# Performance work log

Measured on AMD Instinct MI355X. Metric: run time of the kernel, lower is better.

The kernel has to match this reference:

```python
import jax, jax.numpy as jnp
import numpy as np

EMBED_DIM = 1024
ATTN_DIM = 1024


def setup_inputs() -> dict:
    key = jax.random.key(0)
    k1, k2, k3, k4 = jax.random.split(key, 4)
    embedded = jax.random.normal(k1, (4, 2048, EMBED_DIM), dtype=jnp.float32)
    # torch nn.Linear weights are [out_features, in_features]
    s = 1.0 / np.sqrt(EMBED_DIM)
    Wk = jax.random.uniform(k2, (ATTN_DIM, EMBED_DIM), jnp.float32, -s, s)
    Wq = jax.random.uniform(k3, (ATTN_DIM, EMBED_DIM), jnp.float32, -s, s)
    Wv = jax.random.uniform(k4, (ATTN_DIM, EMBED_DIM), jnp.float32, -s, s)
    return {"embedded": embedded, "Wk": Wk, "Wq": Wq, "Wv": Wv}


def reference(embedded, Wk, Wq, Wv):
    # projections: x @ W.T  (torch Linear, no bias)
    k = jnp.einsum("bse,ae->bsa", embedded, Wk)
    q = jnp.einsum("bse,ae->bsa", embedded, Wq)
    v = jnp.einsum("bse,ae->bsa", embedded, Wv)
    scale = 1.0 / jnp.sqrt(jnp.float32(ATTN_DIM))
    attn = jnp.einsum("bqa,bka->bqk", q, k) * scale  # [B, S, S]
    S = attn.shape[1]
    causal = jnp.tril(jnp.ones((S, S), dtype=bool))
    attn = jnp.where(causal[None, :, :], attn, -jnp.inf)
    a = jax.nn.softmax(attn, axis=2)
    out = jnp.einsum("bqk,bka->bqa", a, v)
    return jnp.round(out, 4)
```

## Files before the change

### kernel.cpp

```cpp
#include <hip/hip_runtime.h>
#include <hip/hip_bf16.h>
#include <stdint.h>

typedef __bf16 bf16_t;
typedef bf16_t bf16x8 __attribute__((ext_vector_type(8)));
typedef bf16_t bf16x4 __attribute__((ext_vector_type(4)));
typedef float f32x4 __attribute__((ext_vector_type(4)));

#define BM 128
#define BN 128
#define BK 32

__device__ __forceinline__ void gload_lds16(const void* g, void* l) {
    __builtin_amdgcn_global_load_lds(
        (const __attribute__((address_space(1))) void*)(uintptr_t)g,
        (__attribute__((address_space(3))) void*)(uintptr_t)l,
        16, 0, 0);
}

template <int EPI>
__device__ __forceinline__ void gemm_body(
    bf16_t* __restrict__ As, bf16_t* __restrict__ Bs,
    const bf16_t* __restrict__ A, long lda,
    const bf16_t* __restrict__ B, long ldb,
    void* __restrict__ Cv, long ldc,
    int k0beg, int k1end, float scale, int m0, int n0,
    float* __restrict__ rs, int use_atomic)
{
    const int tid = threadIdx.x;
    const int wid = tid >> 6, lane = tid & 63;
    const int wr = wid >> 1, wc = wid & 1;
    const int hw = lane >> 4, ln = lane & 15;

    const bf16_t *srcA[2], *srcB[2];
#pragma unroll
    for (int i = 0; i < 2; i++) {
        const int c = tid + i * 256;
        const int row = c >> 2;
        const int j = ((c & 3) - (row >> 1)) & 3;
        srcA[i] = A + (size_t)(m0 + row) * lda + j * 8;
        srcB[i] = B + (size_t)(n0 + row) * ldb + j * 8;
    }

    f32x4 acc[4][4] = {};

    for (int k0 = k0beg; k0 < k1end; k0 += BK) {
        gload_lds16(srcA[0] + k0, &As[wid * 512]);
        gload_lds16(srcA[1] + k0, &As[2048 + wid * 512]);
        gload_lds16(srcB[0] + k0, &Bs[wid * 512]);
        gload_lds16(srcB[1] + k0, &Bs[2048 + wid * 512]);
        __syncthreads();

        bf16x8 af[4], bfr[4];
#pragma unroll
        for (int t = 0; t < 4; t++) {
            const int r  = wr * 64 + t * 16 + ln;
            const int rb = wc * 64 + t * 16 + ln;
            af[t]  = *(const bf16x8*)&As[r  * BK + (((hw + (r  >> 1)) & 3) * 8)];
            bfr[t] = *(const bf16x8*)&Bs[rb * BK + (((hw + (rb >> 1)) & 3) * 8)];
        }
#pragma unroll
        for (int ti = 0; ti < 4; ti++)
#pragma unroll
            for (int tj = 0; tj < 4; tj++)
                acc[ti][tj] = __builtin_amdgcn_mfma_f32_16x16x32_bf16(
                    af[ti], bfr[tj], acc[ti][tj], 0, 0, 0);
        __syncthreads();
    }

#pragma unroll
    for (int ti = 0; ti < 4; ti++) {
        const int rbase = m0 + wr * 64 + ti * 16 + hw * 4;
        f32x4 inv4;
        if (EPI == 2) {
            const float4 r4 = *(const float4*)&rs[rbase];
            inv4[0] = 1.0f / r4.x; inv4[1] = 1.0f / r4.y;
            inv4[2] = 1.0f / r4.z; inv4[3] = 1.0f / r4.w;
        }
        float part[4] = {0.f, 0.f, 0.f, 0.f};
#pragma unroll
        for (int tj = 0; tj < 4; tj++) {
            const int col = n0 + wc * 64 + tj * 16 + ln;
            if (EPI == 4) {
                const int bb = rbase >> 11;
                const int s  = rbase & 2047;
                const int d  = col - 2048;
                bf16x4 o;
#pragma unroll
                for (int rg = 0; rg < 4; rg++) o[rg] = (bf16_t)acc[ti][tj][rg];
                *(bf16x4*)&((bf16_t*)Cv)[(size_t)bb * 2097152 + (size_t)d * 2048 + s] = o;
            } else {
#pragma unroll
                for (int rg = 0; rg < 4; rg++) {
                    const size_t idx = (size_t)(rbase + rg) * ldc + col;
                    if (EPI == 0) {
                        ((bf16_t*)Cv)[idx] = (bf16_t)(acc[ti][tj][rg]);
                    } else if (EPI == 2) {
                        const float v = acc[ti][tj][rg] * inv4[rg];
                        if (use_atomic) atomicAdd(&((float*)Cv)[idx], v);
                        else            ((float*)Cv)[idx] = v;
                    } else {
                        const float e = (col <= rbase + rg)
                                      ? __expf(acc[ti][tj][rg] * scale) : 0.0f;
                        part[rg] += e;
                        ((bf16_t*)Cv)[idx] = (bf16_t)e;
                    }
                }
            }
        }
        if (EPI == 3) {
#pragma unroll
            for (int rg = 0; rg < 4; rg++) {
                float p = part[rg];
                p += __shfl_xor(p, 1, 64);
                p += __shfl_xor(p, 2, 64);
                p += __shfl_xor(p, 4, 64);
                p += __shfl_xor(p, 8, 64);
                if (ln == 0) atomicAdd(&rs[rbase + rg], p);
            }
        }
    }
}

__global__ __launch_bounds__(256) void gemm1_qkv(
    const bf16_t* __restrict__ xb, const bf16_t* __restrict__ Wb,
    bf16_t* __restrict__ QKVb, bf16_t* __restrict__ Vt)
{
    __shared__ __align__(16) bf16_t As[BM * BK];
    __shared__ __align__(16) bf16_t Bs[BN * BK];
    const int lin = blockIdx.x;
    const int xcd = lin & 7;
    const int j   = lin >> 3;
    const int p   = j >> 6;
    const int w   = j & 63;
    const int mblk = xcd * 8 + (w >> 3);
    const int nblk = p * 8 + (w & 7);
    const int m0 = mblk * BM, n0 = nblk * BN;
    if (nblk < 16)
        gemm_body<0>(As, Bs, xb, 1024, Wb, 1024, QKVb, 2048,
                     0, 1024, 1.0f, m0, n0, nullptr, 0);
    else
        gemm_body<4>(As, Bs, xb, 1024, Wb, 1024, Vt, 2048,
                     0, 1024, 1.0f, m0, n0, nullptr, 0);
}

__global__ __launch_bounds__(256) void qk_gemm(
    const bf16_t* __restrict__ QKVb, bf16_t* __restrict__ E,
    float* __restrict__ rowsum)
{
    __shared__ __align__(16) bf16_t As[BM * BK];
    __shared__ __align__(16) bf16_t Bs[BN * BK];
    const int b = blockIdx.x & 3;
    int rem = blockIdx.x >> 2;
    int my = 15, nx = 0;
#pragma unroll
    for (int m = 15; m >= 0; --m) {
        if (rem < m + 1) { my = m; nx = rem; break; }
        rem -= m + 1;
    }
    const bf16_t* base = QKVb + (size_t)b * (2048L * 2048);
    gemm_body<3>(As, Bs,
                 base + 1024, 2048,
                 base, 2048,
                 E + (size_t)b * (2048L * 2048), 2048,
                 0, 1024, 0.03125f, my * BM, nx * BN,
                 rowsum + b * 2048, 0);
}

__global__ __launch_bounds__(256) void gemm3_pv(
    const bf16_t* __restrict__ E, const bf16_t* __restrict__ Vt,
    const float* __restrict__ rowsum, float* __restrict__ out)
{
    __shared__ __align__(16) bf16_t As[BM * BK];
    __shared__ __align__(16) bf16_t Bs[BN * BK];
    const int b = blockIdx.x & 3;
    const int item = blockIdx.x >> 2;
    int s, nx, k0, k1, at;
    if (item < 64) {
        s = item >> 3; nx = item & 7;
        k0 = 0; k1 = (s + 1) * 128; at = 0;
    } else {
        const int q = item - 64;
        s = 8 + (q >> 4);
        const int r = q & 15;
        const int ci = r >> 3;
        nx = r & 7;
        k0 = ci ? 1024 : 0;
        k1 = ci ? (s + 1) * 128 : 1024;
        at = 1;
    }
    gemm_body<2>(As, Bs,
                 E + (size_t)b * (2048L * 2048), 2048,
                 Vt + (size_t)b * (1024L * 2048), 2048,
                 out + (size_t)b * (2048L * 1024), 1024,
                 k0, k1, 1.0f, s * BM, nx * BN,
                 (float*)rowsum + b * 2048, at);
}

__global__ __launch_bounds__(256) void cast_all(
    const float* __restrict__ x,
    const float* __restrict__ Wk, const float* __restrict__ Wq,
    const float* __restrict__ Wv,
    bf16_t* __restrict__ xb, bf16_t* __restrict__ Wb,
    float* __restrict__ rowsum, float* __restrict__ out)
{
    const int blk = blockIdx.x;
    if (blk >= 11272) {
        const int v = blk - 11272;
        const size_t off = (size_t)(v >> 10) * 2097152 + 1048576
                         + (size_t)(v & 1023) * 1024 + (size_t)threadIdx.x * 4;
        *(float4*)(out + off) = make_float4(0.f, 0.f, 0.f, 0.f);
        return;
    }
    if (blk >= 11264) {
        const size_t i = ((size_t)(blk - 11264) * 256 + threadIdx.x) * 4;
        *(float4*)(rowsum + i) = make_float4(0.f, 0.f, 0.f, 0.f);
        return;
    }
    const float* src;
    bf16_t* dst;
    if (blk < 8192) {
        const size_t i = ((size_t)blk * 256 + threadIdx.x) * 4;
        src = x + i;
        dst = xb + i;
    } else {
        const size_t j = ((size_t)(blk - 8192) * 256 + threadIdx.x) * 4;
        dst = Wb + j;
        if (j < (size_t)1048576)      src = Wk + j;
        else if (j < (size_t)2097152) src = Wq + (j - 1048576);
        else                          src = Wv + (j - 2097152);
    }
    const float4 v = *(const float4*)src;
    bf16x4 o;
    o.x = (bf16_t)v.x; o.y = (bf16_t)v.y; o.z = (bf16_t)v.z; o.w = (bf16_t)v.w;
    *(bf16x4*)dst = o;
}

extern "C" void kernel_launch(void* const* d_in, const int* in_sizes, int n_in,
                              void* d_out, int out_size, void* d_ws, size_t ws_size,
                              hipStream_t stream)
{
    const float* x  = (const float*)d_in[0];
    const float* Wk = (const float*)d_in[1];
    const float* Wq = (const float*)d_in[2];
    const float* Wv = (const float*)d_in[3];
    char* ws = (char*)d_ws;

    bf16_t* QKVb   = (bf16_t*)(ws);
    bf16_t* Vt     = (bf16_t*)(ws + ((size_t)32 << 20));
    bf16_t* xb     = (bf16_t*)(ws + ((size_t)48 << 20));
    bf16_t* Wb     = (bf16_t*)(ws + ((size_t)64 << 20));
    bf16_t* E      = (bf16_t*)(ws + ((size_t)48 << 20));
    float*  rowsum = (float*)(ws + ((size_t)80 << 20));
    float*  out    = (float*)d_out;

    cast_all<<<15368, 256, 0, stream>>>(x, Wk, Wq, Wv, xb, Wb, rowsum, out);

    gemm1_qkv<<<1536, 256, 0, stream>>>(xb, Wb, QKVb, Vt);

    qk_gemm<<<544, 256, 0, stream>>>(QKVb, E, rowsum);

    gemm3_pv<<<768, 256, 0, stream>>>(E, Vt, rowsum, out);
}
```

Measured before the change: 232.1 us.

## Fuse all four kernels into one persistent kernel with grid barriers

```diff
diff --git a/kernel.cpp b/kernel.cpp
--- a/kernel.cpp
+++ b/kernel.cpp
@@ -10,12 +10,35 @@
 #define BM 128
 #define BN 128
 #define BK 32
+#define NBLK 768
 
 __device__ __forceinline__ void gload_lds16(const void* g, void* l) {
     __builtin_amdgcn_global_load_lds(
         (const __attribute__((address_space(1))) void*)(uintptr_t)g,
         (__attribute__((address_space(3))) void*)(uintptr_t)l,
         16, 0, 0);
+}
+
+__device__ __forceinline__ void grid_barrier(unsigned* cnt, unsigned* gen)
+{
+    __syncthreads();
+    if (threadIdx.x == 0) {
+        const unsigned g = __hip_atomic_load(gen, __ATOMIC_ACQUIRE,
+                                             __HIP_MEMORY_SCOPE_AGENT);
+        const unsigned a = __hip_atomic_fetch_add(cnt, 1u, __ATOMIC_ACQ_REL,
+                                                  __HIP_MEMORY_SCOPE_AGENT);
+        if (a == NBLK - 1u) {
+            __hip_atomic_store(cnt, 0u, __ATOMIC_RELAXED,
+                               __HIP_MEMORY_SCOPE_AGENT);
+            __hip_atomic_fetch_add(gen, 1u, __ATOMIC_ACQ_REL,
+                                   __HIP_MEMORY_SCOPE_AGENT);
+        } else {
+            while (__hip_atomic_load(gen, __ATOMIC_ACQUIRE,
+                                     __HIP_MEMORY_SCOPE_AGENT) == g)
+                __builtin_amdgcn_s_sleep(8);
+        }
+    }
+    __syncthreads();
 }
 
 template <int EPI>
@@ -122,118 +145,112 @@
     }
 }
 
-__global__ __launch_bounds__(256) void gemm1_qkv(
-    const bf16_t* __restrict__ xb, const bf16_t* __restrict__ Wb,
-    bf16_t* __restrict__ QKVb, bf16_t* __restrict__ Vt)
-{
-    __shared__ __align__(16) bf16_t As[BM * BK];
-    __shared__ __align__(16) bf16_t Bs[BN * BK];
-    const int lin = blockIdx.x;
-    const int xcd = lin & 7;
-    const int j   = lin >> 3;
-    const int p   = j >> 6;
-    const int w   = j & 63;
-    const int mblk = xcd * 8 + (w >> 3);
-    const int nblk = p * 8 + (w & 7);
-    const int m0 = mblk * BM, n0 = nblk * BN;
-    if (nblk < 16)
-        gemm_body<0>(As, Bs, xb, 1024, Wb, 1024, QKVb, 2048,
-                     0, 1024, 1.0f, m0, n0, nullptr, 0);
-    else
-        gemm_body<4>(As, Bs, xb, 1024, Wb, 1024, Vt, 2048,
-                     0, 1024, 1.0f, m0, n0, nullptr, 0);
-}
-
-__global__ __launch_bounds__(256) void qk_gemm(
-    const bf16_t* __restrict__ QKVb, bf16_t* __restrict__ E,
-    float* __restrict__ rowsum)
-{
-    __shared__ __align__(16) bf16_t As[BM * BK];
-    __shared__ __align__(16) bf16_t Bs[BN * BK];
-    const int b = blockIdx.x & 3;
-    int rem = blockIdx.x >> 2;
-    int my = 15, nx = 0;
-#pragma unroll
-    for (int m = 15; m >= 0; --m) {
-        if (rem < m + 1) { my = m; nx = rem; break; }
-        rem -= m + 1;
-    }
-    const bf16_t* base = QKVb + (size_t)b * (2048L * 2048);
-    gemm_body<3>(As, Bs,
-                 base + 1024, 2048,
-                 base, 2048,
-                 E + (size_t)b * (2048L * 2048), 2048,
-                 0, 1024, 0.03125f, my * BM, nx * BN,
-                 rowsum + b * 2048, 0);
-}
-
-__global__ __launch_bounds__(256) void gemm3_pv(
-    const bf16_t* __restrict__ E, const bf16_t* __restrict__ Vt,
-    const float* __restrict__ rowsum, float* __restrict__ out)
-{
-    __shared__ __align__(16) bf16_t As[BM * BK];
-    __shared__ __align__(16) bf16_t Bs[BN * BK];
-    const int b = blockIdx.x & 3;
-    const int item = blockIdx.x >> 2;
-    int s, nx, k0, k1, at;
-    if (item < 64) {
-        s = item >> 3; nx = item & 7;
-        k0 = 0; k1 = (s + 1) * 128; at = 0;
-    } else {
-        const int q = item - 64;
-        s = 8 + (q >> 4);
-        const int r = q & 15;
-        const int ci = r >> 3;
-        nx = r & 7;
-        k0 = ci ? 1024 : 0;
-        k1 = ci ? (s + 1) * 128 : 1024;
-        at = 1;
-    }
-    gemm_body<2>(As, Bs,
-                 E + (size_t)b * (2048L * 2048), 2048,
-                 Vt + (size_t)b * (1024L * 2048), 2048,
-                 out + (size_t)b * (2048L * 1024), 1024,
-                 k0, k1, 1.0f, s * BM, nx * BN,
-                 (float*)rowsum + b * 2048, at);
-}
-
-__global__ __launch_bounds__(256) void cast_all(
+__global__ __launch_bounds__(256, 3) void mega(
     const float* __restrict__ x,
     const float* __restrict__ Wk, const float* __restrict__ Wq,
     const float* __restrict__ Wv,
     bf16_t* __restrict__ xb, bf16_t* __restrict__ Wb,
-    float* __restrict__ rowsum, float* __restrict__ out)
-{
-    const int blk = blockIdx.x;
-    if (blk >= 11272) {
-        const int v = blk - 11272;
-        const size_t off = (size_t)(v >> 10) * 2097152 + 1048576
-                         + (size_t)(v & 1023) * 1024 + (size_t)threadIdx.x * 4;
-        *(float4*)(out + off) = make_float4(0.f, 0.f, 0.f, 0.f);
-        return;
-    }
-    if (blk >= 11264) {
-        const size_t i = ((size_t)(blk - 11264) * 256 + threadIdx.x) * 4;
-        *(float4*)(rowsum + i) = make_float4(0.f, 0.f, 0.f, 0.f);
-        return;
-    }
-    const float* src;
-    bf16_t* dst;
-    if (blk < 8192) {
-        const size_t i = ((size_t)blk * 256 + threadIdx.x) * 4;
-        src = x + i;
-        dst = xb + i;
-    } else {
-        const size_t j = ((size_t)(blk - 8192) * 256 + threadIdx.x) * 4;
-        dst = Wb + j;
-        if (j < (size_t)1048576)      src = Wk + j;
-        else if (j < (size_t)2097152) src = Wq + (j - 1048576);
-        else                          src = Wv + (j - 2097152);
-    }
-    const float4 v = *(const float4*)src;
-    bf16x4 o;
-    o.x = (bf16_t)v.x; o.y = (bf16_t)v.y; o.z = (bf16_t)v.z; o.w = (bf16_t)v.w;
-    *(bf16x4*)dst = o;
+    bf16_t* __restrict__ QKVb, bf16_t* __restrict__ Vt,
+    bf16_t* __restrict__ E, float* __restrict__ rowsum,
+    float* __restrict__ out, unsigned* __restrict__ bar)
+{
+    __shared__ __align__(16) bf16_t As[BM * BK];
+    __shared__ __align__(16) bf16_t Bs[BN * BK];
+    const int tid = threadIdx.x;
+    unsigned* cnt = bar;
+    unsigned* gen = bar + 1;
+
+    for (int u = blockIdx.x; u < 15368; u += NBLK) {
+        if (u < 8192) {
+            const size_t i = ((size_t)u * 256 + tid) * 4;
+            const float4 v = *(const float4*)(x + i);
+            bf16x4 o;
+            o[0] = (bf16_t)v.x; o[1] = (bf16_t)v.y;
+            o[2] = (bf16_t)v.z; o[3] = (bf16_t)v.w;
+            *(bf16x4*)(xb + i) = o;
+        } else if (u < 11264) {
+            const size_t j = ((size_t)(u - 8192) * 256 + tid) * 4;
+            const float* src;
+            if (j < (size_t)1048576)      src = Wk + j;
+            else if (j < (size_t)2097152) src = Wq + (j - 1048576);
+            else                          src = Wv + (j - 2097152);
+            const float4 v = *(const float4*)src;
+            bf16x4 o;
+            o[0] = (bf16_t)v.x; o[1] = (bf16_t)v.y;
+            o[2] = (bf16_t)v.z; o[3] = (bf16_t)v.w;
+            *(bf16x4*)(Wb + j) = o;
+        } else if (u < 11272) {
+            const size_t i = ((size_t)(u - 11264) * 256 + tid) * 4;
+            *(float4*)(rowsum + i) = make_float4(0.f, 0.f, 0.f, 0.f);
+        } else {
+            const int v = u - 11272;
+            const size_t off = (size_t)(v >> 10) * 2097152 + 1048576
+                             + (size_t)(v & 1023) * 1024 + (size_t)tid * 4;
+            *(float4*)(out + off) = make_float4(0.f, 0.f, 0.f, 0.f);
+        }
+    }
+    grid_barrier(cnt, gen);
+
+    for (int t = blockIdx.x; t < 1536; t += NBLK) {
+        const int xcd = t & 7;
+        const int j   = t >> 3;
+        const int p   = j >> 6;
+        const int w   = j & 63;
+        const int mblk = xcd * 8 + (w >> 3);
+        const int nblk = p * 8 + (w & 7);
+        const int m0 = mblk * BM, n0 = nblk * BN;
+        if (nblk < 16)
+            gemm_body<0>(As, Bs, xb, 1024, Wb, 1024, QKVb, 2048,
+                         0, 1024, 1.0f, m0, n0, nullptr, 0);
+        else
+            gemm_body<4>(As, Bs, xb, 1024, Wb, 1024, Vt, 2048,
+                         0, 1024, 1.0f, m0, n0, nullptr, 0);
+    }
+    grid_barrier(cnt, gen);
+
+    if (blockIdx.x < 544) {
+        const int b = blockIdx.x & 3;
+        int rem = blockIdx.x >> 2;
+        int my = 15, nx = 0;
+#pragma unroll
+        for (int m = 15; m >= 0; --m) {
+            if (rem < m + 1) { my = m; nx = rem; break; }
+            rem -= m + 1;
+        }
+        const bf16_t* base = QKVb + (size_t)b * (2048L * 2048);
+        gemm_body<3>(As, Bs,
+                     base + 1024, 2048,
+                     base, 2048,
+                     E + (size_t)b * (2048L * 2048), 2048,
+                     0, 1024, 0.03125f, my * BM, nx * BN,
+                     rowsum + b * 2048, 0);
+    }
+    grid_barrier(cnt, gen);
+
+    {
+        const int b = blockIdx.x & 3;
+        const int item = blockIdx.x >> 2;
+        int s, nx, k0, k1, at;
+        if (item < 64) {
+            s = item >> 3; nx = item & 7;
+            k0 = 0; k1 = (s + 1) * 128; at = 0;
+        } else {
+            const int q = item - 64;
+            s = 8 + (q >> 4);
+            const int r = q & 15;
+            const int ci = r >> 3;
+            nx = r & 7;
+            k0 = ci ? 1024 : 0;
+            k1 = ci ? (s + 1) * 128 : 1024;
+            at = 1;
+        }
+        gemm_body<2>(As, Bs,
+                     E + (size_t)b * (2048L * 2048), 2048,
+                     Vt + (size_t)b * (1024L * 2048), 2048,
+                     out + (size_t)b * (2048L * 1024), 1024,
+                     k0, k1, 1.0f, s * BM, nx * BN,
+                     rowsum + b * 2048, at);
+    }
 }
 
 extern "C" void kernel_launch(void* const* d_in, const int* in_sizes, int n_in,
@@ -246,19 +263,16 @@
     const float* Wv = (const float*)d_in[3];
     char* ws = (char*)d_ws;
 
-    bf16_t* QKVb   = (bf16_t*)(ws);
-    bf16_t* Vt     = (bf16_t*)(ws + ((size_t)32 << 20));
-    bf16_t* xb     = (bf16_t*)(ws + ((size_t)48 << 20));
-    bf16_t* Wb     = (bf16_t*)(ws + ((size_t)64 << 20));
-    bf16_t* E      = (bf16_t*)(ws + ((size_t)48 << 20));
-    float*  rowsum = (float*)(ws + ((size_t)80 << 20));
-    float*  out    = (float*)d_out;
-
-    cast_all<<<15368, 256, 0, stream>>>(x, Wk, Wq, Wv, xb, Wb, rowsum, out);
-
-    gemm1_qkv<<<1536, 256, 0, stream>>>(xb, Wb, QKVb, Vt);
-
-    qk_gemm<<<544, 256, 0, stream>>>(QKVb, E, rowsum);
-
-    gemm3_pv<<<768, 256, 0, stream>>>(E, Vt, rowsum, out);
-}
+    bf16_t*   QKVb   = (bf16_t*)(ws);
+    bf16_t*   Vt     = (bf16_t*)(ws + ((size_t)32 << 20));
+    bf16_t*   xb     = (bf16_t*)(ws + ((size_t)48 << 20));
+    bf16_t*   Wb     = (bf16_t*)(ws + ((size_t)64 << 20));
+    bf16_t*   E      = (bf16_t*)(ws + ((size_t)48 << 20));
+    float*    rowsum = (float*)(ws + ((size_t)80 << 20));
+    unsigned* bar    = (unsigned*)(ws + ((size_t)81 << 20));
+    float*    out    = (float*)d_out;
+
+    hipMemsetAsync(bar, 0, 2 * sizeof(unsigned), stream);
+    mega<<<NBLK, 256, 0, stream>>>(x, Wk, Wq, Wv, xb, Wb, QKVb, Vt, E,
+                                   rowsum, out, bar);
+}
```

New measurement: 729.7 us. 3.14x slower.
